# Kernel optimization log

Measured on AMD Instinct MI355X. Metric: run time of the kernel, lower is better.

## Reference

```python
import jax, jax.numpy as jnp
import numpy as np

# Module/config constants (match init_kwargs and torch forward defaults, octaves=8)
H, W, B = 1024, 1024, 16
OCTAVES = 8
PERSISTENCE = 0.5
LACUNARITY = 2.0
EXPONENT = 4.0
SCALE = 100.0
EVOLUTION = 0.1
FRAME = 0
BRIGHTNESS = 0.0
CONTRAST = 0.0
MIN_CLAMP = 0.0
MAX_CLAMP = 1.0
P_COUNT = max(H, W) ** 2  # permutation table size (doubled via concat)


def _fade(t):
    # 6t^5 - 15t^4 + 10t^3, Horner form
    return t * t * t * (t * (t * 6.0 - 15.0) + 10.0)


def _lerp(t, a, b):
    return a + t * (b - a)


def _grad(h, x, y, z):
    h = h & 15
    u = jnp.where(h < 8, x, y)
    v = jnp.where(h < 4, y, jnp.where((h == 12) | (h == 14), x, z))
    return jnp.where((h & 1) == 0, u, -u) + jnp.where((h & 2) == 0, v, -v)


def _noise(x, y, z, p):
    # classic 3D Perlin noise; x:(1,W), y:(H,1), z:(1,) broadcast to (H,W)
    Xi = (jnp.floor(x) % 255).astype(jnp.int32)
    Yi = (jnp.floor(y) % 255).astype(jnp.int32)
    Zi = (jnp.floor(z) % 255).astype(jnp.int32)
    xf = x - jnp.floor(x)
    yf = y - jnp.floor(y)
    zf = z - jnp.floor(z)
    u = _fade(xf)
    v = _fade(yf)
    w = _fade(zf)
    A = p[Xi] + Yi            # (H,W)
    AA = p[A] + Zi
    AB = p[A + 1] + Zi
    Bc = p[Xi + 1] + Yi
    BA = p[Bc] + Zi
    BB = p[Bc + 1] + Zi
    x1 = _lerp(u, _grad(p[AA], xf, yf, zf), _grad(p[BA], xf - 1, yf, zf))
    x2 = _lerp(u, _grad(p[AB], xf, yf - 1, zf), _grad(p[BB], xf - 1, yf - 1, zf))
    x3 = _lerp(u, _grad(p[AA + 1], xf, yf, zf - 1), _grad(p[BA + 1], xf - 1, yf, zf - 1))
    x4 = _lerp(u, _grad(p[AB + 1], xf, yf - 1, zf - 1), _grad(p[BB + 1], xf - 1, yf - 1, zf - 1))
    return _lerp(w, _lerp(v, x1, x2), _lerp(v, x3, x4))


def _forward(p_all, X, Y, Z):
    xs = jnp.arange(W, dtype=jnp.float32)[None, :] + X  # (1,W)
    ys = jnp.arange(H, dtype=jnp.float32)[:, None] + Y  # (H,1)

    def one_image(p, b):
        z0 = EVOLUTION * b + Z + FRAME  # (1,)
        acc = jnp.zeros((H, W), jnp.float32)
        for o in range(OCTAVES):  # small fixed loop over octaves
            freq = LACUNARITY ** o
            amp = PERSISTENCE ** o
            nz = (z0 + FRAME * EVOLUTION) / SCALE * freq
            n = _noise(xs / SCALE * freq, ys / SCALE * freq, nz, p)
            # noise * amp**exponent accumulated with weight amp -> amp**(exponent+1)
            acc = acc + n * np.float32(amp ** EXPONENT * amp)
        mn, mx = acc.min(), acc.max()
        img = (acc - mn) / (mx - mn) * (MAX_CLAMP - MIN_CLAMP) + MIN_CLAMP
        # second range_normalize(x) with None targets is the identity
        return (img + BRIGHTNESS) * (1.0 + CONTRAST)

    imgs = jax.vmap(one_image)(p_all, jnp.arange(B, dtype=jnp.float32))  # (B,H,W)
    return imgs[..., None]  # (B,H,W,1)


def setup_inputs() -> dict:
    key = jax.random.key(0)
    keys = jax.random.split(key, B)
    perm = jax.vmap(lambda k: jax.random.permutation(k, P_COUNT))(keys).astype(jnp.int32)
    p_all = jnp.concatenate([perm, perm], axis=1)  # (B, 2*P_COUNT), torch .repeat(2)
    kx, ky, kz = jax.random.split(jax.random.fold_in(key, 1), 3)
    X = jax.random.uniform(kx, (1,), jnp.float32, 0.0, 1000.0)
    Y = jax.random.uniform(ky, (1,), jnp.float32, 0.0, 1000.0)
    Z = jax.random.uniform(kz, (1,), jnp.float32, 0.0, 100.0)
    return {"p_all": p_all, "X": X, "Y": Y, "Z": Z}


def reference(p_all, X, Y, Z):
    return _forward(p_all, X, Y, Z)
```

## Files before the change

### kernel.cpp

```cpp
#include <hip/hip_runtime.h>


#define HW  1048576
#define PSTRIDE 2097152
#define PBS 1049088
#define OCT 4
#define RPB 8

struct ZTab { float zf, w; int Zi, pad; float w0, w1, wz0, wz1; };

__device__ __forceinline__ float fadef(float t) {
    return t * t * t * (t * (t * 6.0f - 15.0f) + 10.0f);
}
__device__ __forceinline__ void gdec(int h, float& a, float& cy, float& cz) {
    float s1 = (h & 1) ? -1.f : 1.f;
    float s2 = (h & 2) ? -1.f : 1.f;
    bool  vx = (h == 12) || (h == 14);
    a  = ((h < 8) ? s1 : 0.f) + (vx ? s2 : 0.f);
    cy = ((h >= 8) ? s1 : 0.f) + ((h < 4) ? s2 : 0.f);
    cz = (h >= 4 && !vx) ? s2 : 0.f;
}

__constant__ const float AW[8] = {
    1.0f, 0.03125f, 9.765625e-4f, 3.0517578125e-5f,
    9.5367431640625e-7f, 2.9802322387695312e-8f,
    9.313225746154785e-10f, 2.9103830456733704e-11f
};

__global__ void ppf_k0(const float* __restrict__ Z, ZTab* __restrict__ zs) {
    int t = threadIdx.x;
    if (t < 128) {
        int b = t >> 3, o = t & 7;
        float z0 = 0.1f * (float)b + Z[0];
        float freq = (float)(1 << o);
        float nz = (z0 / 100.0f) * freq;
        float fz = floorf(nz);
        ZTab zt;
        zt.Zi = ((int)fz) % 255;
        zt.zf = nz - fz;
        zt.w  = fadef(zt.zf);
        zt.pad = 0;
        zt.w0 = 1.0f - zt.w;
        zt.w1 = zt.w;
        zt.wz0 = zt.w0 * zt.zf;
        zt.wz1 = zt.w1 * (zt.zf - 1.0f);
        zs[t] = zt;
    }
}

__global__ void ppf_k0b(const int* __restrict__ p_all, unsigned char* __restrict__ pbp) {
    int L = blockIdx.x;
    int b = L & 15;
    int idx = (L >> 4) * 256 + threadIdx.x;
    if (idx < PBS / 4) {
        const int* p = p_all + (size_t)b * PSTRIDE;
        int4 v = ((const int4*)p)[idx];
        int n4 = p[idx * 4 + 4];
        uchar4 o;
        o.x = (unsigned char)((v.x & 15) | ((v.y & 15) << 4));
        o.y = (unsigned char)((v.y & 15) | ((v.z & 15) << 4));
        o.z = (unsigned char)((v.z & 15) | ((v.w & 15) << 4));
        o.w = (unsigned char)((v.w & 15) | ((n4 & 15) << 4));
        ((uchar4*)(pbp + (size_t)b * PBS))[idx] = o;
    }
}

template <int USE_PBP>
__global__ void ppf_k1(const int* __restrict__ p_all, const unsigned char* __restrict__ pbp,
                       const ZTab* __restrict__ zs, unsigned* __restrict__ G2) {
    int L = blockIdx.x;
    int b = L & 15;
    int i = L >> 4;
    int j = threadIdx.x;
    const int* p = p_all + (size_t)b * PSTRIDE;
    int pi = p[i];
    int q  = p[pi + j];
    const unsigned char* pp = pbp + (size_t)b * PBS;
    unsigned w = 0;
#pragma unroll
    for (int o = 0; o < OCT; o++) {
        int Zi = zs[b * 8 + o].Zi;
        unsigned byt;
        if (USE_PBP) {
            byt = pp[q + Zi];
        } else {
            byt = (unsigned)((p[q + Zi] & 15) | ((p[q + Zi + 1] & 15) << 4));
        }
        w |= byt << (8 * o);
    }
    G2[((size_t)b << 16) + ((unsigned)j << 8) + (unsigned)i] = w;
}

__launch_bounds__(256, 8)
__global__ void ppf_k2(const unsigned* __restrict__ G2,
                       const ZTab* __restrict__ zs,
                       const float* __restrict__ X, const float* __restrict__ Y,
                       float* __restrict__ out, float2* __restrict__ pmm) {
    __shared__ __align__(16) float2 CT[2][OCT * 256];
    __shared__ float red[8];

    const int tid = threadIdx.x;
    const int L = blockIdx.x;
    const int b = L & 15, bx = L >> 4;
    const float X0 = X[0], Y0 = Y[0];

    float zw0[OCT], zw1[OCT], zwz0[OCT], zwz1[OCT];
#pragma unroll
    for (int o = 0; o < OCT; o++) {
        ZTab z = zs[b * 8 + o];
        zw0[o] = z.w0; zw1[o] = z.w1; zwz0[o] = z.wz0; zwz1[o] = z.wz1;
    }

    float txs[4];
#pragma unroll
    for (int i = 0; i < 4; i++) txs[i] = ((float)(tid + 256 * i) + X0) * 0.01f;

    const unsigned* gb = G2 + ((size_t)b << 16);

    unsigned g0r[OCT], g1r[OCT];
    int prevYi[OCT];
#pragma unroll
    for (int o = 0; o < OCT; o++) prevYi[o] = -1;

    float mnr = 1e30f, mxr = -1e30f;
    int cur = 0;

    for (int rr = 0; rr < RPB; rr++) {
        const int r = bx * RPB + rr;
        const float ty = ((float)r + Y0) * 0.01f;

#pragma unroll
        for (int o = 0; o < OCT; o++) {
            float y  = ty * (float)(1 << o);
            float fy = floorf(y);
            float yf = y - fy, ym1 = yf - 1.0f;
            float v  = fadef(yf);
            int Yi = (int)fy;
            if (Yi != prevYi[o]) {
                const unsigned* grow = gb + ((unsigned)Yi << 8) + tid;
                g0r[o] = grow[0];
                g1r[o] = grow[256];
                prevYi[o] = Yi;
            }
            int byt0 = (g0r[o] >> (8 * o)) & 255;
            int byt1 = (g1r[o] >> (8 * o)) & 255;
            float a0, cy0, cz0, a1, cy1, cz1;
            gdec(byt0 & 15, a0, cy0, cz0);
            gdec(byt0 >> 4, a1, cy1, cz1);
            float A_0  = fmaf(zw1[o],  a1,  zw0[o] * a0);
            float CY_0 = fmaf(zw1[o],  cy1, zw0[o] * cy0);
            float CZ_0 = fmaf(zwz1[o], cz1, zwz0[o] * cz0);
            gdec(byt1 & 15, a0, cy0, cz0);
            gdec(byt1 >> 4, a1, cy1, cz1);
            float A_1  = fmaf(zw1[o],  a1,  zw0[o] * a0);
            float CY_1 = fmaf(zw1[o],  cy1, zw0[o] * cy0);
            float CZ_1 = fmaf(zwz1[o], cz1, zwz0[o] * cz0);
            float CA = A_0 + v * (A_1 - A_0);
            float B0 = fmaf(CY_0, yf,  CZ_0);
            float B1 = fmaf(CY_1, ym1, CZ_1);
            float CB = B0 + v * (B1 - B0);
            float aw = AW[o];
            CT[cur][o * 256 + tid] = make_float2(CA * aw, CB * aw);
        }
        __syncthreads();

        float accv[4] = {0.f, 0.f, 0.f, 0.f};
#pragma unroll
        for (int o = 0; o < OCT; o++) {
            const float fr = (float)(1 << o);
            const float2* cto = CT[cur] + o * 256;
            float xfv[4], uv[4];
            float2 c0v[4], c1v[4];
#pragma unroll
            for (int i = 0; i < 4; i++) {
                float x  = txs[i] * fr;
                float fx = floorf(x);
                float xf = x - fx;
                int  s   = (int)fx;
                xfv[i] = xf;
                uv[i]  = fadef(xf);
                c0v[i] = cto[s];
                c1v[i] = cto[s + 1];
            }
#pragma unroll
            for (int i = 0; i < 4; i++) {
                float P = fmaf(c0v[i].x, xfv[i], c0v[i].y);
                float Q = fmaf(c1v[i].x, xfv[i] - 1.0f, c1v[i].y);
                accv[i] += fmaf(uv[i], Q - P, P);
            }
        }

        size_t obase = ((size_t)b << 20) + ((size_t)r << 10) + tid;
#pragma unroll
        for (int i = 0; i < 4; i++) out[obase + 256 * i] = accv[i];
        mnr = fminf(mnr, fminf(fminf(accv[0], accv[1]), fminf(accv[2], accv[3])));
        mxr = fmaxf(mxr, fmaxf(fmaxf(accv[0], accv[1]), fmaxf(accv[2], accv[3])));

        cur ^= 1;
    }

#pragma unroll
    for (int off = 32; off > 0; off >>= 1) {
        mnr = fminf(mnr, __shfl_down(mnr, off));
        mxr = fmaxf(mxr, __shfl_down(mxr, off));
    }
    if ((tid & 63) == 0) { red[2 * (tid >> 6)] = mnr; red[2 * (tid >> 6) + 1] = mxr; }
    __syncthreads();
    if (tid == 0) {
        float mn = fminf(fminf(red[0], red[2]), fminf(red[4], red[6]));
        float mx = fmaxf(fmaxf(red[1], red[3]), fmaxf(red[5], red[7]));
        pmm[b * 128 + bx] = make_float2(mn, mx);
    }
}

__global__ void ppf_k3(float* __restrict__ out, const float2* __restrict__ pmm) {
    __shared__ float sred[8];
    __shared__ float sbc[2];
    int b = blockIdx.y;
    int tid = threadIdx.x;

    float mn = 1e30f, mx = -1e30f;
    if (tid < 128) { float2 v = pmm[b * 128 + tid]; mn = v.x; mx = v.y; }
#pragma unroll
    for (int off = 32; off > 0; off >>= 1) {
        mn = fminf(mn, __shfl_down(mn, off));
        mx = fmaxf(mx, __shfl_down(mx, off));
    }
    if ((tid & 63) == 0) { sred[2 * (tid >> 6)] = mn; sred[2 * (tid >> 6) + 1] = mx; }
    __syncthreads();
    if (tid == 0) {
        mn = fminf(fminf(sred[0], sred[2]), fminf(sred[4], sred[6]));
        mx = fmaxf(fmaxf(sred[1], sred[3]), fmaxf(sred[5], sred[7]));
        sbc[0] = mn;
        sbc[1] = 1.0f / (mx - mn);
    }
    __syncthreads();
    float bmn = sbc[0], bs = sbc[1];

    int idx = blockIdx.x * 256 + tid;
    float4* o4 = (float4*)(out + (size_t)b * HW);
    float4 v = o4[idx];
    v.x = (v.x - bmn) * bs;
    v.y = (v.y - bmn) * bs;
    v.z = (v.z - bmn) * bs;
    v.w = (v.w - bmn) * bs;
    o4[idx] = v;
}

extern "C" void kernel_launch(void* const* d_in, const int* in_sizes, int n_in,
                              void* d_out, int out_size, void* d_ws, size_t ws_size,
                              hipStream_t stream) {
    const int*   p_all = (const int*)d_in[0];
    const float* X     = (const float*)d_in[1];
    const float* Y     = (const float*)d_in[2];
    const float* Z     = (const float*)d_in[3];
    float* out = (float*)d_out;
    char* ws = (char*)d_ws;

    const size_t GSZ = (size_t)16 * 65536 * 4;
    const size_t OFF_PBP = GSZ;
    const size_t OFF_ZS_FULL = OFF_PBP + (size_t)16 * PBS;
    const size_t NEED_FULL   = OFF_ZS_FULL + 8192 + 16384;
    bool full = (ws_size >= NEED_FULL);
    size_t off_zs = full ? OFF_ZS_FULL : OFF_PBP;

    unsigned* G2       = (unsigned*)ws;
    unsigned char* pbp = (unsigned char*)(ws + OFF_PBP);
    ZTab*   zs         = (ZTab*)  (ws + off_zs);
    float2* pmm        = (float2*)(ws + off_zs + 8192);

    ppf_k0<<<1, 128, 0, stream>>>(Z, zs);
    if (full) {
        ppf_k0b<<<16400, 256, 0, stream>>>(p_all, pbp);
        ppf_k1<1><<<4096, 256, 0, stream>>>(p_all, pbp, zs, G2);
    } else {
        ppf_k1<0><<<4096, 256, 0, stream>>>(p_all, pbp, zs, G2);
    }
    ppf_k2<<<2048, 256, 0, stream>>>(G2, zs, X, Y, out, pmm);
    ppf_k3<<<dim3(1024, 16), 256, 0, stream>>>(out, pmm);
}
```

Baseline: 333.7 us.

## Fuse noise compute and normalization via cooperative grid sync, keeping rows in registers

Replaces the separate noise kernel and normalization kernel with one cooperative kernel. Each block computes 16 rows and holds them in registers, publishes per-block min/max, synchronizes the whole grid, then writes normalized output once. This removes the extra read-modify-write pass over the 64 MB output and one launch. The costs are higher register pressure (launch bounds cut to 4 blocks per CU), a grid-wide barrier, and a requirement that all 1024 blocks be co-resident; if the cooperative launch fails it falls back to the old two-kernel path.

```diff
diff --git a/kernel.cpp b/kernel.cpp
--- a/kernel.cpp
+++ b/kernel.cpp
@@ -1,4 +1,5 @@
 #include <hip/hip_runtime.h>
+#include <hip/hip_cooperative_groups.h>
 
 
 #define HW  1048576
@@ -6,6 +7,9 @@
 #define PBS 1049088
 #define OCT 4
 #define RPB 8
+#define RPB2 16
+
+namespace cg = cooperative_groups;
 
 struct ZTab { float zf, w; int Zi, pad; float w0, w1, wz0, wz1; };
 
@@ -91,6 +95,156 @@
     G2[((size_t)b << 16) + ((unsigned)j << 8) + (unsigned)i] = w;
 }
 
+__device__ __forceinline__ void ct_build_row(
+        float ty, int tid, const unsigned* gb,
+        const float* zw0, const float* zw1, const float* zwz0, const float* zwz1,
+        unsigned* g0r, unsigned* g1r, int* prevYi, float2* ctcur) {
+#pragma unroll
+    for (int o = 0; o < OCT; o++) {
+        float y  = ty * (float)(1 << o);
+        float fy = floorf(y);
+        float yf = y - fy, ym1 = yf - 1.0f;
+        float v  = fadef(yf);
+        int Yi = (int)fy;
+        if (Yi != prevYi[o]) {
+            const unsigned* grow = gb + ((unsigned)Yi << 8) + tid;
+            g0r[o] = grow[0];
+            g1r[o] = grow[256];
+            prevYi[o] = Yi;
+        }
+        int byt0 = (g0r[o] >> (8 * o)) & 255;
+        int byt1 = (g1r[o] >> (8 * o)) & 255;
+        float a0, cy0, cz0, a1, cy1, cz1;
+        gdec(byt0 & 15, a0, cy0, cz0);
+        gdec(byt0 >> 4, a1, cy1, cz1);
+        float A_0  = fmaf(zw1[o],  a1,  zw0[o] * a0);
+        float CY_0 = fmaf(zw1[o],  cy1, zw0[o] * cy0);
+        float CZ_0 = fmaf(zwz1[o], cz1, zwz0[o] * cz0);
+        gdec(byt1 & 15, a0, cy0, cz0);
+        gdec(byt1 >> 4, a1, cy1, cz1);
+        float A_1  = fmaf(zw1[o],  a1,  zw0[o] * a0);
+        float CY_1 = fmaf(zw1[o],  cy1, zw0[o] * cy0);
+        float CZ_1 = fmaf(zwz1[o], cz1, zwz0[o] * cz0);
+        float CA = A_0 + v * (A_1 - A_0);
+        float B0 = fmaf(CY_0, yf,  CZ_0);
+        float B1 = fmaf(CY_1, ym1, CZ_1);
+        float CB = B0 + v * (B1 - B0);
+        float aw = AW[o];
+        ctcur[o * 256 + tid] = make_float2(CA * aw, CB * aw);
+    }
+}
+
+__device__ __forceinline__ void pixel_row(const float2* ctcur, const float* txs,
+                                          float* accv) {
+#pragma unroll
+    for (int o = 0; o < OCT; o++) {
+        const float fr = (float)(1 << o);
+        const float2* cto = ctcur + o * 256;
+        float xfv[4], uv[4];
+        float2 c0v[4], c1v[4];
+#pragma unroll
+        for (int i = 0; i < 4; i++) {
+            float x  = txs[i] * fr;
+            float fx = floorf(x);
+            float xf = x - fx;
+            int  s   = (int)fx;
+            xfv[i] = xf;
+            uv[i]  = fadef(xf);
+            c0v[i] = cto[s];
+            c1v[i] = cto[s + 1];
+        }
+#pragma unroll
+        for (int i = 0; i < 4; i++) {
+            float P = fmaf(c0v[i].x, xfv[i], c0v[i].y);
+            float Q = fmaf(c1v[i].x, xfv[i] - 1.0f, c1v[i].y);
+            accv[i] += fmaf(uv[i], Q - P, P);
+        }
+    }
+}
+
+__launch_bounds__(256, 4)
+__global__ void ppf_k2f(const unsigned* __restrict__ G2,
+                        const ZTab* __restrict__ zs,
+                        const float* __restrict__ X, const float* __restrict__ Y,
+                        float* __restrict__ out, float2* __restrict__ pmm) {
+    __shared__ __align__(16) float2 CT[2][OCT * 256];
+    __shared__ float red[8];
+    __shared__ float sbc[2];
+
+    const int tid = threadIdx.x;
+    const int L = blockIdx.x;
+    const int b = L & 15, bx = L >> 4;
+    const float X0 = X[0], Y0 = Y[0];
+
+    float zw0[OCT], zw1[OCT], zwz0[OCT], zwz1[OCT];
+#pragma unroll
+    for (int o = 0; o < OCT; o++) {
+        ZTab z = zs[b * 8 + o];
+        zw0[o] = z.w0; zw1[o] = z.w1; zwz0[o] = z.wz0; zwz1[o] = z.wz1;
+    }
+
+    float txs[4];
+#pragma unroll
+    for (int i = 0; i < 4; i++) txs[i] = ((float)(tid + 256 * i) + X0) * 0.01f;
+
+    const unsigned* gb = G2 + ((size_t)b << 16);
+    unsigned g0r[OCT], g1r[OCT];
+    int prevYi[OCT];
+#pragma unroll
+    for (int o = 0; o < OCT; o++) prevYi[o] = -1;
+
+    float acc[RPB2][4];
+    float mnr = 1e30f, mxr = -1e30f;
+
+#pragma unroll
+    for (int rr = 0; rr < RPB2; rr++) {
+        const int cur = rr & 1;
+        const float ty = ((float)(bx * RPB2 + rr) + Y0) * 0.01f;
+        ct_build_row(ty, tid, gb, zw0, zw1, zwz0, zwz1, g0r, g1r, prevYi, CT[cur]);
+        __syncthreads();
+        acc[rr][0] = acc[rr][1] = acc[rr][2] = acc[rr][3] = 0.f;
+        pixel_row(CT[cur], txs, acc[rr]);
+        mnr = fminf(mnr, fminf(fminf(acc[rr][0], acc[rr][1]), fminf(acc[rr][2], acc[rr][3])));
+        mxr = fmaxf(mxr, fmaxf(fmaxf(acc[rr][0], acc[rr][1]), fmaxf(acc[rr][2], acc[rr][3])));
+    }
+
+#pragma unroll
+    for (int off = 32; off > 0; off >>= 1) {
+        mnr = fminf(mnr, __shfl_down(mnr, off));
+        mxr = fmaxf(mxr, __shfl_down(mxr, off));
+    }
+    if ((tid & 63) == 0) { red[2 * (tid >> 6)] = mnr; red[2 * (tid >> 6) + 1] = mxr; }
+    __syncthreads();
+    if (tid == 0) {
+        float mn = fminf(fminf(red[0], red[2]), fminf(red[4], red[6]));
+        float mx = fmaxf(fmaxf(red[1], red[3]), fmaxf(red[5], red[7]));
+        pmm[b * 64 + bx] = make_float2(mn, mx);
+    }
+    __threadfence();
+    cg::this_grid().sync();
+
+    if (tid < 64) {
+        float2 v = pmm[b * 64 + tid];
+        float mn = v.x, mx = v.y;
+#pragma unroll
+        for (int off = 32; off > 0; off >>= 1) {
+            mn = fminf(mn, __shfl_down(mn, off));
+            mx = fmaxf(mx, __shfl_down(mx, off));
+        }
+        if (tid == 0) { sbc[0] = mn; sbc[1] = 1.0f / (mx - mn); }
+    }
+    __syncthreads();
+    const float bmn = sbc[0], bs = sbc[1];
+
+#pragma unroll
+    for (int rr = 0; rr < RPB2; rr++) {
+        size_t obase = ((size_t)b << 20) + ((size_t)(bx * RPB2 + rr) << 10) + tid;
+#pragma unroll
+        for (int i = 0; i < 4; i++)
+            out[obase + 256 * i] = (acc[rr][i] - bmn) * bs;
+    }
+}
+
 __launch_bounds__(256, 8)
 __global__ void ppf_k2(const unsigned* __restrict__ G2,
                        const ZTab* __restrict__ zs,
@@ -110,13 +264,11 @@
         ZTab z = zs[b * 8 + o];
         zw0[o] = z.w0; zw1[o] = z.w1; zwz0[o] = z.wz0; zwz1[o] = z.wz1;
     }
-
     float txs[4];
 #pragma unroll
     for (int i = 0; i < 4; i++) txs[i] = ((float)(tid + 256 * i) + X0) * 0.01f;
 
     const unsigned* gb = G2 + ((size_t)b << 16);
-
     unsigned g0r[OCT], g1r[OCT];
     int prevYi[OCT];
 #pragma unroll
@@ -124,81 +276,20 @@
 
     float mnr = 1e30f, mxr = -1e30f;
     int cur = 0;
-
     for (int rr = 0; rr < RPB; rr++) {
         const int r = bx * RPB + rr;
         const float ty = ((float)r + Y0) * 0.01f;
-
-#pragma unroll
-        for (int o = 0; o < OCT; o++) {
-            float y  = ty * (float)(1 << o);
-            float fy = floorf(y);
-            float yf = y - fy, ym1 = yf - 1.0f;
-            float v  = fadef(yf);
-            int Yi = (int)fy;
-            if (Yi != prevYi[o]) {
-                const unsigned* grow = gb + ((unsigned)Yi << 8) + tid;
-                g0r[o] = grow[0];
-                g1r[o] = grow[256];
-                prevYi[o] = Yi;
-            }
-            int byt0 = (g0r[o] >> (8 * o)) & 255;
-            int byt1 = (g1r[o] >> (8 * o)) & 255;
-            float a0, cy0, cz0, a1, cy1, cz1;
-            gdec(byt0 & 15, a0, cy0, cz0);
-            gdec(byt0 >> 4, a1, cy1, cz1);
-            float A_0  = fmaf(zw1[o],  a1,  zw0[o] * a0);
-            float CY_0 = fmaf(zw1[o],  cy1, zw0[o] * cy0);
-            float CZ_0 = fmaf(zwz1[o], cz1, zwz0[o] * cz0);
-            gdec(byt1 & 15, a0, cy0, cz0);
-            gdec(byt1 >> 4, a1, cy1, cz1);
-            float A_1  = fmaf(zw1[o],  a1,  zw0[o] * a0);
-            float CY_1 = fmaf(zw1[o],  cy1, zw0[o] * cy0);
-            float CZ_1 = fmaf(zwz1[o], cz1, zwz0[o] * cz0);
-            float CA = A_0 + v * (A_1 - A_0);
-            float B0 = fmaf(CY_0, yf,  CZ_0);
-            float B1 = fmaf(CY_1, ym1, CZ_1);
-            float CB = B0 + v * (B1 - B0);
-            float aw = AW[o];
-            CT[cur][o * 256 + tid] = make_float2(CA * aw, CB * aw);
-        }
+        ct_build_row(ty, tid, gb, zw0, zw1, zwz0, zwz1, g0r, g1r, prevYi, CT[cur]);
         __syncthreads();
-
         float accv[4] = {0.f, 0.f, 0.f, 0.f};
-#pragma unroll
-        for (int o = 0; o < OCT; o++) {
-            const float fr = (float)(1 << o);
-            const float2* cto = CT[cur] + o * 256;
-            float xfv[4], uv[4];
-            float2 c0v[4], c1v[4];
-#pragma unroll
-            for (int i = 0; i < 4; i++) {
-                float x  = txs[i] * fr;
-                float fx = floorf(x);
-                float xf = x - fx;
-                int  s   = (int)fx;
-                xfv[i] = xf;
-                uv[i]  = fadef(xf);
-                c0v[i] = cto[s];
-                c1v[i] = cto[s + 1];
-            }
-#pragma unroll
-            for (int i = 0; i < 4; i++) {
-                float P = fmaf(c0v[i].x, xfv[i], c0v[i].y);
-                float Q = fmaf(c1v[i].x, xfv[i] - 1.0f, c1v[i].y);
-                accv[i] += fmaf(uv[i], Q - P, P);
-            }
-        }
-
+        pixel_row(CT[cur], txs, accv);
         size_t obase = ((size_t)b << 20) + ((size_t)r << 10) + tid;
 #pragma unroll
         for (int i = 0; i < 4; i++) out[obase + 256 * i] = accv[i];
         mnr = fminf(mnr, fminf(fminf(accv[0], accv[1]), fminf(accv[2], accv[3])));
         mxr = fmaxf(mxr, fmaxf(fmaxf(accv[0], accv[1]), fmaxf(accv[2], accv[3])));
-
         cur ^= 1;
     }
-
 #pragma unroll
     for (int off = 32; off > 0; off >>= 1) {
         mnr = fminf(mnr, __shfl_down(mnr, off));
@@ -218,7 +309,6 @@
     __shared__ float sbc[2];
     int b = blockIdx.y;
     int tid = threadIdx.x;
-
     float mn = 1e30f, mx = -1e30f;
     if (tid < 128) { float2 v = pmm[b * 128 + tid]; mn = v.x; mx = v.y; }
 #pragma unroll
@@ -236,7 +326,6 @@
     }
     __syncthreads();
     float bmn = sbc[0], bs = sbc[1];
-
     int idx = blockIdx.x * 256 + tid;
     float4* o4 = (float4*)(out + (size_t)b * HW);
     float4 v = o4[idx];
@@ -276,6 +365,16 @@
     } else {
         ppf_k1<0><<<4096, 256, 0, stream>>>(p_all, pbp, zs, G2);
     }
-    ppf_k2<<<2048, 256, 0, stream>>>(G2, zs, X, Y, out, pmm);
-    ppf_k3<<<dim3(1024, 16), 256, 0, stream>>>(out, pmm);
-}
+
+    const unsigned* G2c = G2; const ZTab* zsc = zs;
+    const float* Xc = X; const float* Yc = Y;
+    float* outc = out; float2* pmmc = pmm;
+    void* args[6] = { (void*)&G2c, (void*)&zsc, (void*)&Xc, (void*)&Yc,
+                      (void*)&outc, (void*)&pmmc };
+    hipError_t e = hipLaunchCooperativeKernel((void*)ppf_k2f, dim3(1024),
+                                              dim3(256), args, 0, stream);
+    if (e != hipSuccess) {
+        ppf_k2<<<2048, 256, 0, stream>>>(G2, zs, X, Y, out, pmm);
+        ppf_k3<<<dim3(1024, 16), 256, 0, stream>>>(out, pmm);
+    }
+}
```

New measurement: 1.187 ms. +255.6%, slower.
